# Kernel optimization log

Measured on AMD Instinct MI355X. Metric: run time of the kernel, lower is better.

## Reference

```python
import jax, jax.numpy as jnp
import numpy as np

BATCH = 8192
IN_FEATURES = 128
OUT_FEATURES = 256
GRID_SIZE = 20
ORDER = 3
L = GRID_SIZE + ORDER  # coeffs length per edge = 23


def setup_inputs() -> dict:
    key = jax.random.key(0)
    kx, kc = jax.random.split(key)
    x = jax.random.normal(kx, (BATCH, IN_FEATURES), dtype=jnp.float32)
    # fused per-edge B-spline coefficients: [out_features, in_features, grid_size+order]
    coeffs = jax.random.normal(kc, (OUT_FEATURES, IN_FEATURES, L), dtype=jnp.float32) * 0.1
    return {"x": x, "coeffs": coeffs}


def reference(x, coeffs):
    # x: [B, I], coeffs: [O, I, L]
    O, I, Lc = coeffs.shape
    B = x.shape[0]
    s = jax.nn.sigmoid(x)                      # x_clamped in (0, 1)
    idx = s * (GRID_SIZE - 1)                  # fractional bin index in [0, 19)
    k = idx.astype(jnp.int32)                  # trunc == floor since idx >= 0
    w1 = idx - k.astype(x.dtype)
    w0 = 1.0 - w1
    k0 = jnp.clip(k, 0, Lc - 1)                # [B, I]
    k1 = jnp.clip(k + 1, 0, Lc - 1)
    # Build sparse interpolation weights [B, I, L] (two nonzeros per (b, j)),
    # then contract against the shared coefficient tensor in one fused reduce:
    # out[b, i] = sum_j c[i, j, k0[b,j]] * w0[b,j] + c[i, j, k1[b,j]] * w1[b,j]
    brow = jnp.arange(B)[:, None]
    jcol = jnp.arange(I)[None, :]
    W = jnp.zeros((B, I, Lc), dtype=x.dtype)
    W = W.at[brow, jcol, k0].add(w0)
    W = W.at[brow, jcol, k1].add(w1)
    return jnp.einsum('bjl,ijl->bi', W, coeffs)  # [B, O]
```

## Files before the change

kernel.cpp:

```cpp
#include <hip/hip_runtime.h>
#include <hip/hip_fp16.h>

#define BATCH 8192
#define IN_F 128
#define OUT_F 256
#define LC 23
#define BROW 768
#define JPW 32

typedef _Float16 f16x8 __attribute__((ext_vector_type(8)));
typedef float f32x4 __attribute__((ext_vector_type(4)));
typedef _Float16 half2v __attribute__((ext_vector_type(2)));

__global__ __launch_bounds__(256) void prep_kernel(
    const float* __restrict__ coeffs, _Float16* __restrict__ cp2) {
    int t = blockIdx.x * 256 + threadIdx.x;
    int col = t & 15;
    int u = t >> 4;
    int q = u % 3;
    int v = u / 3;
    int g = v & 15;
    int j = v >> 4;
    int i = g * 16 + col;
    int s0 = q * 8;
    const float* src = coeffs + ((size_t)i * IN_F + j) * LC;
    f16x8 w;
#pragma unroll
    for (int e = 0; e < 8; ++e) {
        int s = s0 + e;
        float f = (s < 20) ? src[s] : 0.0f;
        w[e] = (_Float16)f;
    }
    char* dst = reinterpret_cast<char*>(cp2) +
                (size_t)(j * 16 + g) * BROW + q * 256 + col * 16;
    *reinterpret_cast<f16x8*>(dst) = w;
}

__global__ __launch_bounds__(256, 2) void kan_mfma6(
    const float* __restrict__ x, const char* __restrict__ cp2,
    float* __restrict__ out) {
    __shared__ uint2 mlds[IN_F][64];

    const int tid = threadIdx.x;
    const int lane = tid & 63;
    const int ks = tid >> 6;
    const int l15 = lane & 15;
    const int q = lane >> 4;

    int wg = (blockIdx.x & 7) * 64 + (blockIdx.x >> 3);
    const int mb = wg >> 2;
    const int bn = wg & 3;
    const int b0 = mb * 64;

    {
        const int row = tid & 63;
        const int jb = (tid >> 6) * 32;
        const float4* xr = reinterpret_cast<const float4*>(
            x + (size_t)(b0 + row) * IN_F + jb);
#pragma unroll
        for (int u = 0; u < 8; ++u) {
            float4 xv = xr[u];
#pragma unroll
            for (int e = 0; e < 4; ++e) {
                float xvv = (e == 0) ? xv.x : (e == 1) ? xv.y
                           : (e == 2) ? xv.z : xv.w;
                float s = 1.0f / (1.0f + __expf(-xvv));
                float idxf = s * 19.0f;
                int k = (int)idxf;
                k = (k > 18) ? 18 : k;
                float w1 = idxf - (float)k;
                float w0 = 1.0f - w1;
                unsigned u0 = __half_as_ushort(__float2half(w0));
                unsigned u1 = __half_as_ushort(__float2half(w1));
                unsigned lo, hi;
                if (k & 1) { lo = u0 << 16; hi = u1; }
                else       { lo = u0 | (u1 << 16); hi = 0u; }
                unsigned P = (unsigned)(k >> 1);
                mlds[jb + u * 4 + e][row] = uint2{lo, hi | (P << 16)};
            }
        }
    }
    __syncthreads();

    const int j0 = ks * JPW;
    const char* bbase = cp2 + (size_t)(bn * 4) * BROW + q * 256 + l15 * 16;

    f32x4 acc[4][4];
#pragma unroll
    for (int mf = 0; mf < 4; ++mf)
#pragma unroll
        for (int nf = 0; nf < 4; ++nf) acc[mf][nf] = f32x4{0.f, 0.f, 0.f, 0.f};

    uint4 bcur[4] = {uint4{0, 0, 0, 0}, uint4{0, 0, 0, 0},
                     uint4{0, 0, 0, 0}, uint4{0, 0, 0, 0}};
    if (q < 3) {
#pragma unroll
        for (int nf = 0; nf < 4; ++nf)
            bcur[nf] = *reinterpret_cast<const uint4*>(
                bbase + (size_t)(j0 * 16 + nf) * BROW);
    }

#pragma unroll 4
    for (int jj = 0; jj < JPW; ++jj) {
        const int jn = j0 + ((jj + 1) & (JPW - 1));
        uint4 bnx[4] = {uint4{0, 0, 0, 0}, uint4{0, 0, 0, 0},
                        uint4{0, 0, 0, 0}, uint4{0, 0, 0, 0}};
        if (q < 3) {
#pragma unroll
            for (int nf = 0; nf < 4; ++nf)
                bnx[nf] = *reinterpret_cast<const uint4*>(
                    bbase + (size_t)(jn * 16 + nf) * BROW);
        }
        const int jabs = j0 + jj;
#pragma unroll
        for (int mf = 0; mf < 4; ++mf) {
            uint2 m = mlds[jabs][mf * 16 + l15];
            unsigned lo = m.x;
            unsigned hi = m.y & 0xFFFFu;
            int d = (int)(m.y >> 16) - q * 4;
            union { uint32_t u[4]; f16x8 h; } au;
#pragma unroll
            for (int r = 0; r < 4; ++r) {
                uint32_t v = (d == r) ? lo : 0u;
                v = (d == r - 1) ? hi : v;
                au.u[r] = v;
            }
            union { uint4 v; f16x8 h; } bu;
#pragma unroll
            for (int nf = 0; nf < 4; ++nf) {
                bu.v = bcur[nf];
                acc[mf][nf] = __builtin_amdgcn_mfma_f32_16x16x32_f16(
                    au.h, bu.h, acc[mf][nf], 0, 0, 0);
            }
        }
#pragma unroll
        for (int nf = 0; nf < 4; ++nf) bcur[nf] = bnx[nf];
    }

    __syncthreads();
    float* red = reinterpret_cast<float*>(&mlds[0][0]);
#pragma unroll
    for (int mf = 0; mf < 4; ++mf) {
#pragma unroll
        for (int nf = 0; nf < 4; ++nf) {
#pragma unroll
            for (int r = 0; r < 4; ++r)
                red[ks * 4096 + (mf * 16 + q * 4 + r) * 64 + nf * 16 + l15] =
                    acc[mf][nf][r];
        }
    }
    __syncthreads();
#pragma unroll
    for (int it = 0; it < 16; ++it) {
        int idx = it * 256 + tid;
        float s = red[idx] + red[4096 + idx] + red[8192 + idx] +
                  red[12288 + idx];
        int row = idx >> 6;
        int col = idx & 63;
        out[(size_t)(b0 + row) * OUT_F + bn * 64 + col] = s;
    }
}

__device__ __forceinline__ float dot2_acc(unsigned cbits, unsigned wbits,
                                          float acc) {
#if __has_builtin(__builtin_amdgcn_fdot2)
    union { unsigned u; half2v h; } c, w;
    c.u = cbits; w.u = wbits;
    return __builtin_amdgcn_fdot2(c.h, w.h, acc, false);
#else
    __half2 hc = *reinterpret_cast<const __half2*>(&cbits);
    __half2 hw = *reinterpret_cast<const __half2*>(&wbits);
    float2 fc = __half22float2(hc);
    float2 fw = __half22float2(hw);
    return acc + fc.x * fw.x + fc.y * fw.y;
#endif
}

__global__ __launch_bounds__(256) void build_ctg_kernel(
    const float* __restrict__ coeffs, unsigned short* __restrict__ ctg) {
    int tid = blockIdx.x * 256 + threadIdx.x;
    int qq = tid & 63;
    int k = (tid >> 6) % LC;
    int j = tid / (64 * LC);
    if (j >= IN_F) return;
    int k1 = (k + 1 < LC) ? (k + 1) : (LC - 1);
    union { unsigned short h[8]; uint4 v; } u;
#pragma unroll
    for (int c = 0; c < 4; ++c) {
        int i = qq * 4 + c;
        const float* base = coeffs + ((size_t)i * IN_F + j) * LC;
        u.h[2 * c]     = __half_as_ushort(__float2half(base[k]));
        u.h[2 * c + 1] = __half_as_ushort(__float2half(base[k1]));
    }
    reinterpret_cast<uint4*>(ctg)[tid] = u.v;
}

__global__ __launch_bounds__(256) void kan_main_kernel(
    const float* __restrict__ x, const char* __restrict__ ctg,
    float* __restrict__ out) {
    __shared__ unsigned metas[4][2 * IN_F];
    const int wave = threadIdx.x >> 6;
    const int lane = threadIdx.x & 63;
    const int b = blockIdx.x * 4 + wave;
    float2 xv = reinterpret_cast<const float2*>(x + (size_t)b * IN_F)[lane];
    uint4 m;
#pragma unroll
    for (int t = 0; t < 2; ++t) {
        float xs = t ? xv.y : xv.x;
        float s = 1.0f / (1.0f + __expf(-xs));
        float idxf = s * 19.0f;
        int k = (int)idxf;
        k = (k > 18) ? 18 : k;
        float w1 = idxf - (float)k;
        float w0 = 1.0f - w1;
        int j = 2 * lane + t;
        unsigned off = (unsigned)((j * LC + k) << 10);
        half2v w; w[0] = (_Float16)w0; w[1] = (_Float16)w1;
        unsigned wbits = *reinterpret_cast<unsigned*>(&w);
        if (t == 0) { m.x = off; m.y = wbits; }
        else        { m.z = off; m.w = wbits; }
    }
    reinterpret_cast<uint4*>(&metas[wave][0])[lane] = m;
    __syncthreads();
    const unsigned lanebase = lane * 16;
    const uint4* mrow = reinterpret_cast<const uint4*>(&metas[wave][0]);
    float acc0 = 0.f, acc1 = 0.f, acc2 = 0.f, acc3 = 0.f;
#pragma unroll 8
    for (int j2 = 0; j2 < IN_F / 2; ++j2) {
        uint4 mm = mrow[j2];
        {
            const uint4 e = *reinterpret_cast<const uint4*>(
                ctg + (size_t)(lanebase + mm.x));
            acc0 = dot2_acc(e.x, mm.y, acc0);
            acc1 = dot2_acc(e.y, mm.y, acc1);
            acc2 = dot2_acc(e.z, mm.y, acc2);
            acc3 = dot2_acc(e.w, mm.y, acc3);
        }
        {
            const uint4 e = *reinterpret_cast<const uint4*>(
                ctg + (size_t)(lanebase + mm.z));
            acc0 = dot2_acc(e.x, mm.w, acc0);
            acc1 = dot2_acc(e.y, mm.w, acc1);
            acc2 = dot2_acc(e.z, mm.w, acc2);
            acc3 = dot2_acc(e.w, mm.w, acc3);
        }
    }
    float4 r = make_float4(acc0, acc1, acc2, acc3);
    reinterpret_cast<float4*>(out + (size_t)b * OUT_F)[lane] = r;
}

extern "C" void kernel_launch(void* const* d_in, const int* in_sizes, int n_in,
                              void* d_out, int out_size, void* d_ws,
                              size_t ws_size, hipStream_t stream) {
    const float* x = (const float*)d_in[0];
    const float* coeffs = (const float*)d_in[1];
    float* out = (float*)d_out;

    const size_t cp2_bytes = (size_t)IN_F * 16 * BROW;
    const size_t ctg_bytes = (size_t)IN_F * LC * 64 * 16;

    if (d_ws != nullptr && ws_size >= cp2_bytes) {
        _Float16* cp2 = (_Float16*)d_ws;
        prep_kernel<<<384, 256, 0, stream>>>(coeffs, cp2);
        kan_mfma6<<<512, 256, 0, stream>>>(x, (const char*)cp2, out);
    } else if (d_ws != nullptr && ws_size >= ctg_bytes) {
        char* ctg = (char*)d_ws;
        const int totalA = IN_F * LC * 64;
        build_ctg_kernel<<<(totalA + 255) / 256, 256, 0, stream>>>(
            coeffs, (unsigned short*)ctg);
        kan_main_kernel<<<BATCH / 4, 256, 0, stream>>>(x, ctg, out);
    } else {
        kan_main_kernel<<<BATCH / 4, 256, 0, stream>>>(x, (const char*)d_ws,
                                                       out);
    }
}
```

Baseline: 34.70 us.

## Widen MFMA block tile to 128 output columns with 8-wave K-split

Result: faster. 31.20 us (-10.1%).

```diff
diff --git a/kernel.cpp b/kernel.cpp
--- a/kernel.cpp
+++ b/kernel.cpp
@@ -6,7 +6,7 @@
 #define OUT_F 256
 #define LC 23
 #define BROW 768
-#define JPW 32
+#define JPW 16
 
 typedef _Float16 f16x8 __attribute__((ext_vector_type(8)));
 typedef float f32x4 __attribute__((ext_vector_type(4)));
@@ -36,7 +36,7 @@
     *reinterpret_cast<f16x8*>(dst) = w;
 }
 
-__global__ __launch_bounds__(256, 2) void kan_mfma6(
+__global__ __launch_bounds__(512, 2) void kan_mfma7(
     const float* __restrict__ x, const char* __restrict__ cp2,
     float* __restrict__ out) {
     __shared__ uint2 mlds[IN_F][64];
@@ -46,19 +46,21 @@
     const int ks = tid >> 6;
     const int l15 = lane & 15;
     const int q = lane >> 4;
-
-    int wg = (blockIdx.x & 7) * 64 + (blockIdx.x >> 3);
-    const int mb = wg >> 2;
-    const int bn = wg & 3;
+    const int q4 = q * 4;
+    const int qc = (q < 3) ? q : 2;
+
+    int wg = (blockIdx.x & 7) * 32 + (blockIdx.x >> 3);
+    const int mb = wg >> 1;
+    const int bn = wg & 1;
     const int b0 = mb * 64;
 
     {
         const int row = tid & 63;
-        const int jb = (tid >> 6) * 32;
+        const int jb = (tid >> 6) * 16;
         const float4* xr = reinterpret_cast<const float4*>(
             x + (size_t)(b0 + row) * IN_F + jb);
 #pragma unroll
-        for (int u = 0; u < 8; ++u) {
+        for (int u = 0; u < 4; ++u) {
             float4 xv = xr[u];
 #pragma unroll
             for (int e = 0; e < 4; ++e) {
@@ -83,81 +85,88 @@
     __syncthreads();
 
     const int j0 = ks * JPW;
-    const char* bbase = cp2 + (size_t)(bn * 4) * BROW + q * 256 + l15 * 16;
-
-    f32x4 acc[4][4];
+    const char* bbase = cp2 + (size_t)(bn * 8) * BROW + qc * 256 + l15 * 16;
+    auto bld = [&](int j, int nf) {
+        return *reinterpret_cast<const f16x8*>(
+            bbase + (size_t)(j * 16 + nf) * BROW);
+    };
+
+    f32x4 acc[4][8];
 #pragma unroll
     for (int mf = 0; mf < 4; ++mf)
 #pragma unroll
-        for (int nf = 0; nf < 4; ++nf) acc[mf][nf] = f32x4{0.f, 0.f, 0.f, 0.f};
-
-    uint4 bcur[4] = {uint4{0, 0, 0, 0}, uint4{0, 0, 0, 0},
-                     uint4{0, 0, 0, 0}, uint4{0, 0, 0, 0}};
-    if (q < 3) {
-#pragma unroll
-        for (int nf = 0; nf < 4; ++nf)
-            bcur[nf] = *reinterpret_cast<const uint4*>(
-                bbase + (size_t)(j0 * 16 + nf) * BROW);
-    }
-
-#pragma unroll 4
+        for (int nf = 0; nf < 8; ++nf) acc[mf][nf] = f32x4{0.f, 0.f, 0.f, 0.f};
+
+    f16x8 r1[4], r2[4];
+#pragma unroll
+    for (int h = 0; h < 4; ++h) r1[h] = bld(j0, h);
+
+#pragma unroll 2
     for (int jj = 0; jj < JPW; ++jj) {
-        const int jn = j0 + ((jj + 1) & (JPW - 1));
-        uint4 bnx[4] = {uint4{0, 0, 0, 0}, uint4{0, 0, 0, 0},
-                        uint4{0, 0, 0, 0}, uint4{0, 0, 0, 0}};
-        if (q < 3) {
+        const int j = j0 + jj;
+#pragma unroll
+        for (int h = 0; h < 4; ++h) r2[h] = bld(j, 4 + h);
+        f16x8 au[4];
+        {
+            const uint2* mrow = &mlds[j][0];
+#pragma unroll
+            for (int mf = 0; mf < 4; ++mf) {
+                uint2 m = mrow[mf * 16 + l15];
+                unsigned lo = m.x;
+                unsigned hi = m.y & 0xFFFFu;
+                int d = (int)(m.y >> 16) - q4;
+                union { uint32_t u[4]; f16x8 h; } a;
+#pragma unroll
+                for (int r = 0; r < 4; ++r) {
+                    uint32_t v = (d == r) ? lo : 0u;
+                    v = (d == r - 1) ? hi : v;
+                    a.u[r] = v;
+                }
+                au[mf] = a.h;
+            }
+        }
+#pragma unroll
+        for (int mf = 0; mf < 4; ++mf)
 #pragma unroll
             for (int nf = 0; nf < 4; ++nf)
-                bnx[nf] = *reinterpret_cast<const uint4*>(
-                    bbase + (size_t)(jn * 16 + nf) * BROW);
-        }
-        const int jabs = j0 + jj;
-#pragma unroll
-        for (int mf = 0; mf < 4; ++mf) {
-            uint2 m = mlds[jabs][mf * 16 + l15];
-            unsigned lo = m.x;
-            unsigned hi = m.y & 0xFFFFu;
-            int d = (int)(m.y >> 16) - q * 4;
-            union { uint32_t u[4]; f16x8 h; } au;
-#pragma unroll
-            for (int r = 0; r < 4; ++r) {
-                uint32_t v = (d == r) ? lo : 0u;
-                v = (d == r - 1) ? hi : v;
-                au.u[r] = v;
-            }
-            union { uint4 v; f16x8 h; } bu;
-#pragma unroll
-            for (int nf = 0; nf < 4; ++nf) {
-                bu.v = bcur[nf];
                 acc[mf][nf] = __builtin_amdgcn_mfma_f32_16x16x32_f16(
-                    au.h, bu.h, acc[mf][nf], 0, 0, 0);
-            }
-        }
-#pragma unroll
-        for (int nf = 0; nf < 4; ++nf) bcur[nf] = bnx[nf];
+                    au[mf], r1[nf], acc[mf][nf], 0, 0, 0);
+        if (jj + 1 < JPW) {
+#pragma unroll
+            for (int h = 0; h < 4; ++h) r1[h] = bld(j + 1, h);
+        }
+#pragma unroll
+        for (int mf = 0; mf < 4; ++mf)
+#pragma unroll
+            for (int nf = 0; nf < 4; ++nf)
+                acc[mf][4 + nf] = __builtin_amdgcn_mfma_f32_16x16x32_f16(
+                    au[mf], r2[nf], acc[mf][4 + nf], 0, 0, 0);
     }
 
     __syncthreads();
     float* red = reinterpret_cast<float*>(&mlds[0][0]);
 #pragma unroll
-    for (int mf = 0; mf < 4; ++mf) {
-#pragma unroll
-        for (int nf = 0; nf < 4; ++nf) {
-#pragma unroll
-            for (int r = 0; r < 4; ++r)
-                red[ks * 4096 + (mf * 16 + q * 4 + r) * 64 + nf * 16 + l15] =
-                    acc[mf][nf][r];
-        }
-    }
-    __syncthreads();
-#pragma unroll
-    for (int it = 0; it < 16; ++it) {
-        int idx = it * 256 + tid;
-        float s = red[idx] + red[4096 + idx] + red[8192 + idx] +
-                  red[12288 + idx];
-        int row = idx >> 6;
-        int col = idx & 63;
-        out[(size_t)(b0 + row) * OUT_F + bn * 64 + col] = s;
+    for (int pass = 0; pass < 4; ++pass) {
+#pragma unroll
+        for (int mf = 0; mf < 4; ++mf)
+#pragma unroll
+            for (int t = 0; t < 2; ++t)
+#pragma unroll
+                for (int r = 0; r < 4; ++r)
+                    red[ks * 2048 + (mf * 16 + q4 + r) * 32 + t * 16 + l15] =
+                        acc[mf][pass * 2 + t][r];
+        __syncthreads();
+#pragma unroll
+        for (int it = 0; it < 4; ++it) {
+            int idx = it * 512 + tid;
+            float s = 0.f;
+#pragma unroll
+            for (int w = 0; w < 8; ++w) s += red[w * 2048 + idx];
+            int row = idx >> 5;
+            int col = idx & 31;
+            out[(size_t)(b0 + row) * OUT_F + bn * 128 + pass * 32 + col] = s;
+        }
+        __syncthreads();
     }
 }
 
@@ -262,7 +271,7 @@
     if (d_ws != nullptr && ws_size >= cp2_bytes) {
         _Float16* cp2 = (_Float16*)d_ws;
         prep_kernel<<<384, 256, 0, stream>>>(coeffs, cp2);
-        kan_mfma6<<<512, 256, 0, stream>>>(x, (const char*)cp2, out);
+        kan_mfma7<<<256, 512, 0, stream>>>(x, (const char*)cp2, out);
     } else if (d_ws != nullptr && ws_size >= ctg_bytes) {
         char* ctg = (char*)d_ws;
         const int totalA = IN_F * LC * 64;
```
